# Kernel optimization log

Measured on AMD Instinct MI355X. Metric: run time of the kernel, lower is better.

Reference implementation:

```python
import jax, jax.numpy as jnp
import numpy as np

NEG = 0.01  # torch leaky_relu default slope


def conv1d(x, w, pad):
    # x: [B, C, L], w: [O, I, K], stride 1, no bias (as in FC-STGNN extractor)
    return jax.lax.conv_general_dilated(x, w, (1,), [(pad, pad)], dimension_numbers=('NCH', 'OIH', 'NCH'))


def maxpool2(x):
    # MaxPool1d(kernel=2, stride=2, padding=1); torch pads with -inf for max
    return jax.lax.reduce_window(x, -jnp.inf, jax.lax.max, (1, 1, 2), (1, 1, 2), ((0, 0), (0, 0), (1, 1)))


def pos_encoding(n, d):
    # standard sinusoidal PE table, rows 0..n-1 (n <= max_len=5000)
    pos = jnp.arange(n, dtype=jnp.float32)[:, None]
    div = jnp.exp(jnp.arange(0, d, 2, dtype=jnp.float32) * (-float(np.log(10000.0)) / d))
    pe = jnp.zeros((n, d), jnp.float32)
    pe = pe.at[:, 0::2].set(jnp.sin(pos * div))
    pe = pe.at[:, 1::2].set(jnp.cos(pos * div))
    return pe


def mpnn_block(x, gw, gb, bng, bnb, tw, tb):
    # GraphConvpoolMPNN_block_v6 with time_length=1, time_window_size=1, stride=1:
    # one window, decay mask = ones, mean-pool over the size-1 time window is identity.
    bs, two_h, N = x.shape
    X = x.reshape(bs, N, two_h)                                   # (bs*num_windows, num_node*tw, input_dim)
    h = X @ gw + gb                                               # Dot_Graph_Construction mapping
    adj = jnp.einsum('bnd,bmd->bnm', h, h)                        # dot-product adjacency
    eye = jnp.eye(N, dtype=X.dtype)
    adj = jax.nn.leaky_relu(adj - eye * 1e8, NEG)
    adj = jax.nn.softmax(adj, axis=-1) + eye
    Xb = X * bng + bnb                                            # BatchNorm1d eval (running mean 0 / var 1)
    out = jax.nn.leaky_relu(jnp.einsum('bnm,bmd->bnd', adj, Xb) @ tw + tb, NEG)  # MPNN_mk k=1
    return out                                                    # [bs, N, hidden]


def setup_inputs() -> dict:
    key = jax.random.key(0)
    ks = jax.random.split(key, 20)
    bs, D, N = 4, 128, 1024
    H, OUT, KS = 64, 32, 8        # lstmhidden_dim, lstmout_dim, conv_kernel
    HID = 64                      # hidden_dim
    TWOH = 2 * HID
    CONV_OUT = 18
    NCLS = 6
    f32 = jnp.float32
    rn = lambda k, s, sc: jax.random.normal(k, s, f32) * sc
    return {
        'x_enc': rn(ks[0], (bs, D, N), 1.0),
        'x_mark_enc': rn(ks[1], (bs, D, 4), 1.0),
        'x_dec': rn(ks[2], (bs, D // 2, N), 1.0),
        'x_mark_dec': rn(ks[3], (bs, D // 2, 4), 1.0),
        'conv_w1': rn(ks[4], (H, 1, KS), 1.0 / np.sqrt(KS)),
        'bn1_g': jnp.ones((H,), f32), 'bn1_b': jnp.zeros((H,), f32),
        'conv_w2': rn(ks[5], (2 * H, H, KS), 1.0 / np.sqrt(H * KS)),
        'bn2_g': jnp.ones((2 * H,), f32), 'bn2_b': jnp.zeros((2 * H,), f32),
        'conv_w3': rn(ks[6], (OUT, 2 * H, KS), 1.0 / np.sqrt(2 * H * KS)),
        'bn3_g': jnp.ones((OUT,), f32), 'bn3_b': jnp.zeros((OUT,), f32),
        'map2_w': rn(ks[7], (OUT * CONV_OUT, TWOH), 1.0 / np.sqrt(OUT * CONV_OUT)),
        'map2_b': jnp.zeros((TWOH,), f32),
        'map2_bn_g': jnp.ones((TWOH,), f32), 'map2_bn_b': jnp.zeros((TWOH,), f32),
        'g1_w': rn(ks[8], (TWOH, TWOH), 1.0 / np.sqrt(TWOH)), 'g1_b': jnp.zeros((TWOH,), f32),
        'm1_bn_g': jnp.ones((TWOH,), f32), 'm1_bn_b': jnp.zeros((TWOH,), f32),
        't1_w': rn(ks[9], (TWOH, HID), 1.0 / np.sqrt(TWOH)), 't1_b': jnp.zeros((HID,), f32),
        'g2_w': rn(ks[10], (TWOH, TWOH), 1.0 / np.sqrt(TWOH)), 'g2_b': jnp.zeros((TWOH,), f32),
        'm2_bn_g': jnp.ones((TWOH,), f32), 'm2_bn_b': jnp.zeros((TWOH,), f32),
        't2_w': rn(ks[11], (TWOH, HID), 1.0 / np.sqrt(TWOH)), 't2_b': jnp.zeros((HID,), f32),
        'fc1_w': rn(ks[12], (HID * 2 * N, TWOH), 1.0 / np.sqrt(HID * 2 * N)), 'fc1_b': jnp.zeros((TWOH,), f32),
        'fc2_w': rn(ks[13], (TWOH, TWOH), 1.0 / np.sqrt(TWOH)), 'fc2_b': jnp.zeros((TWOH,), f32),
        'fc3_w': rn(ks[14], (TWOH, HID), 1.0 / np.sqrt(TWOH)), 'fc3_b': jnp.zeros((HID,), f32),
        'fc4_w': rn(ks[15], (HID, NCLS), 1.0 / np.sqrt(HID)), 'fc4_b': jnp.zeros((NCLS,), f32),
    }


def reference(x_enc, x_mark_enc, x_dec, x_mark_dec,
              conv_w1, bn1_g, bn1_b, conv_w2, bn2_g, bn2_b, conv_w3, bn3_g, bn3_b,
              map2_w, map2_b, map2_bn_g, map2_bn_b,
              g1_w, g1_b, m1_bn_g, m1_bn_b, t1_w, t1_b,
              g2_w, g2_b, m2_bn_g, m2_bn_b, t2_w, t2_b,
              fc1_w, fc1_b, fc2_w, fc2_b, fc3_w, fc3_b, fc4_w, fc4_b):
    bs, D, N = x_enc.shape
    k = conv_w1.shape[-1]
    # nonlin_map: 1D-CNN feature extractor over each (sample, node) signal
    a = jnp.swapaxes(x_enc.reshape(bs * N, D, 1), 1, 2)           # [bs*N, 1, D]
    a = maxpool2(jax.nn.relu(conv1d(a, conv_w1, k // 2) * bn1_g[None, :, None] + bn1_b[None, :, None]))
    a = maxpool2(jax.nn.relu(conv1d(a, conv_w2, 4) * bn2_g[None, :, None] + bn2_b[None, :, None]))
    a = maxpool2(jax.nn.relu(conv1d(a, conv_w3, 4) * bn3_g[None, :, None] + bn3_b[None, :, None]))
    a = a.reshape(bs * N, -1)                                     # [bs*N, lstmout_dim*conv_out]
    # nonlin_map2: Linear + BatchNorm1d (eval mode affine)
    a = (a @ map2_w + map2_b) * map2_bn_g + map2_bn_b             # [bs*N, 2h]
    two_h = a.shape[-1]
    # positional encoding with the exact reshape/transpose traffic of the torch forward
    x = jnp.swapaxes(a.reshape(bs, N, two_h), 1, 2).reshape(bs * N, two_h)
    x = x + pos_encoding(bs * N, two_h)
    x = jnp.swapaxes(x.reshape(bs, N, two_h), 1, 2)               # [bs, 2h, N]
    # two graph MPNN branches
    o1 = mpnn_block(x, g1_w, g1_b, m1_bn_g, m1_bn_b, t1_w, t1_b)
    o2 = mpnn_block(x, g2_w, g2_b, m2_bn_g, m2_bn_b, t2_w, t2_b)
    f = jnp.concatenate([o1.reshape(bs, -1), o2.reshape(bs, -1)], axis=-1)
    # MLP head
    f = jax.nn.relu(f @ fc1_w + fc1_b)
    f = jax.nn.relu(f @ fc2_w + fc2_b)
    f = jax.nn.relu(f @ fc3_w + fc3_b)
    return f @ fc4_w + fc4_b                                      # [bs, n_class]
```

## Files before the change

kernel.cpp:

```cpp
#include <hip/hip_runtime.h>
#include <hip/hip_bf16.h>
#include <math.h>

#define NEG 0.01f
__device__ __forceinline__ float lrelu(float v){ return v > 0.f ? v : NEG*v; }
__device__ __forceinline__ float frelu(float v){ return v > 0.f ? v : 0.f; }

typedef __attribute__((ext_vector_type(8))) short bf16x8;
typedef __attribute__((ext_vector_type(4))) float f32x4;

__device__ __forceinline__ unsigned short f2bf(float x){
    unsigned int u = __float_as_uint(x);
    unsigned int r = (u + 0x7FFFu + ((u>>16)&1u)) >> 16;
    return (unsigned short)r;
}
__device__ __forceinline__ float bf2f(unsigned short h){
    return __uint_as_float(((unsigned int)h) << 16);
}
__device__ __forceinline__ unsigned short F2B(float x){
    __hip_bfloat16 h = __float2bfloat16(x);
    return *reinterpret_cast<unsigned short*>(&h);
}

__global__ __launch_bounds__(256) void k_prep(const float* __restrict__ w2, const float* __restrict__ w3,
    const float* __restrict__ m2w, const float* __restrict__ t1w, const float* __restrict__ t2w,
    unsigned short* __restrict__ w2s, unsigned short* __restrict__ w3s, unsigned short* __restrict__ m2wbT,
    unsigned short* __restrict__ twThi, unsigned short* __restrict__ twTlo)
{
    int gid = blockIdx.x*256 + threadIdx.x;
    if (gid < 73728) {
        int j = gid / 576, f = gid % 576;
        m2wbT[gid] = f2bf(m2w[f*128 + j]);
    }
    if (gid < 65536) {
        int jj = gid & 7, q = (gid>>3)&3, o = (gid>>5)&127, ks = (gid>>12)&1, k = gid>>13;
        int c = ks*32 + q*8 + jj;
        w2s[gid] = f2bf(w2[o*512 + c*8 + k]);
    }
    if (gid < 32768) {
        int jj = gid & 7, q = (gid>>3)&3, o = (gid>>5)&31, ks = (gid>>10)&3, k = gid>>12;
        int c = ks*32 + q*8 + jj;
        w3s[gid] = f2bf(w3[o*1024 + c*8 + k]);
    }
    if (gid < 16384) {
        int d = gid & 127, e = (gid>>7)&63, br = gid>>13;
        float x = (br ? t2w : t1w)[d*64 + e];
        unsigned short hh = f2bf(x);
        twThi[gid] = hh;
        twTlo[gid] = f2bf(x - bf2f(hh));
    }
}

__global__ __launch_bounds__(256) void k_conv(
    const float* __restrict__ xenc,
    const float* __restrict__ w1, const float* __restrict__ g1, const float* __restrict__ b1,
    const unsigned short* __restrict__ w2s, const float* __restrict__ g2, const float* __restrict__ b2,
    const unsigned short* __restrict__ w3s, const float* __restrict__ g3, const float* __restrict__ b3,
    unsigned short* __restrict__ aflatG)
{
    __shared__ __align__(16) unsigned char smraw[22208];
    float* sigp = (float*)smraw;
    unsigned short* p1T = (unsigned short*)(smraw + 576);
    unsigned short* p2T = (unsigned short*)(smraw + 10304);
    unsigned short* astage = (unsigned short*)(smraw + 21056);

    const int t = threadIdx.x;
    const int s = blockIdx.x;

    {
        unsigned int* zz = (unsigned int*)(smraw + 576);
        for (int i = t; i < 5120; i += 256) zz[i] = 0u;
        if (t < 144) sigp[t] = 0.f;
    }
    __syncthreads();
    if (t < 128) sigp[4 + t] = xenc[(size_t)s*128 + t];
    __syncthreads();

    {
        const int c = t & 63, qg = t >> 6;
        float wr[8];
        #pragma unroll
        for (int k = 0; k < 8; ++k) wr[k] = w1[c*8 + k];
        const float g = g1[c], b = b1[c];
        const int qs = qg*17;
        float win[9];
        {
            int base = 2*qs - 1;
            #pragma unroll
            for (int x = 0; x < 9; ++x) win[x] = (base + x >= 0) ? sigp[base + x] : 0.f;
        }
        #pragma unroll
        for (int j = 0; j < 17; ++j) {
            int q = qs + j;
            float s0 = 0.f, s1 = 0.f;
            #pragma unroll
            for (int k = 0; k < 8; ++k) { s0 += win[k]*wr[k]; s1 += win[k+1]*wr[k]; }
            float v = frelu(s1*g + b);
            if (q > 0) v = fmaxf(v, frelu(s0*g + b));
            if (q < 65) {
                int row = q + 4;
                p1T[row*64 + (((c>>3) ^ (row&7))<<3) + (c&7)] = F2B(v);
            }
            #pragma unroll
            for (int x = 0; x < 7; ++x) win[x] = win[x+2];
            win[7] = sigp[2*q + 8];
            win[8] = sigp[2*q + 9];
        }
    }
    __syncthreads();

    {
        const int wv = t >> 6, l = t & 63, lg = l >> 4, lr = l & 15;
        const int pbase = ((lr & 7) << 1) + (lr >> 3) - 1;
        const int o0 = (wv*2 + 0)*16 + lr;
        const int o1 = (wv*2 + 1)*16 + lr;
        f32x4 acc[2][5] = {};
        #pragma unroll
        for (int k = 0; k < 8; ++k) {
            const int rk = pbase + k;
            const int b0 = rk*64 + ((lg ^ (rk & 7)) << 3);
            #pragma unroll
            for (int ks = 0; ks < 2; ++ks) {
                bf16x8 af0 = *(const bf16x8*)(w2s + ((((k*2 + ks)*128 + o0)*4 + lg)<<3));
                bf16x8 af1 = *(const bf16x8*)(w2s + ((((k*2 + ks)*128 + o1)*4 + lg)<<3));
                const unsigned short* bp = p1T + (ks ? (b0 ^ 32) : b0);
                #pragma unroll
                for (int nt = 0; nt < 5; ++nt) {
                    bf16x8 bfv = *(const bf16x8*)(bp + nt*1024);
                    acc[0][nt] = __builtin_amdgcn_mfma_f32_16x16x32_bf16(af0, bfv, acc[0][nt], 0,0,0);
                    acc[1][nt] = __builtin_amdgcn_mfma_f32_16x16x32_bf16(af1, bfv, acc[1][nt], 0,0,0);
                }
            }
        }
        float ga[2][4], ba[2][4];
        #pragma unroll
        for (int oi = 0; oi < 2; ++oi)
            #pragma unroll
            for (int r = 0; r < 4; ++r) {
                int o = (wv*2 + oi)*16 + lg*4 + r;
                ga[oi][r] = g2[o]; ba[oi][r] = b2[o];
            }
        #pragma unroll
        for (int oi = 0; oi < 2; ++oi)
            #pragma unroll
            for (int nt = 0; nt < 5; ++nt) {
                int p = nt*16 + pbase;
                bool valid = (p >= 0) && (p <= 65);
                float vv[4];
                #pragma unroll
                for (int r = 0; r < 4; ++r) {
                    float v = frelu(acc[oi][nt][r]*ga[oi][r] + ba[oi][r]);
                    vv[r] = valid ? v : -3.0e38f;
                }
                float pv[4];
                #pragma unroll
                for (int r = 0; r < 4; ++r) pv[r] = fmaxf(vv[r], __shfl_xor(vv[r], 8));
                int q = nt*8 + (lr & 7);
                if ((lr >> 3) == 0 && q < 34) {
                    int row2 = q + 4;
                    int o0e = (wv*2 + oi)*16 + lg*4;
                    uint2 pk;
                    pk.x = (unsigned int)F2B(pv[0]) | ((unsigned int)F2B(pv[1]) << 16);
                    pk.y = (unsigned int)F2B(pv[2]) | ((unsigned int)F2B(pv[3]) << 16);
                    *(uint2*)&p2T[row2*128 + (((o0e>>3) ^ (row2&15))<<3) + (o0e&7)] = pk;
                }
            }
    }
    __syncthreads();

    {
        const int wv = t >> 6, l = t & 63, lg = l >> 4, lr = l & 15;
        const int ot = wv & 1, ntb = (wv >> 1) * 2;
        const int ncnt = (wv < 2) ? 2 : 1;
        const int pbase = ((lr & 7) << 1) + (lr >> 3) - 1;
        const int o = ot*16 + lr;
        f32x4 acc[2] = {};
        #pragma unroll
        for (int k = 0; k < 8; ++k) {
            const int rk = pbase + k;
            const int r15 = rk & 15;
            const int c2 = r15 >> 2;
            const int base0 = rk*128 + ((lg ^ (r15 & 3)) << 3) + ntb*2048;
            #pragma unroll
            for (int ks = 0; ks < 4; ++ks) {
                bf16x8 af = *(const bf16x8*)(w3s + ((((k*4 + ks)*32 + o)*4 + lg)<<3));
                const int bb = base0 + (((ks ^ c2) & 3) << 5);
                #pragma unroll
                for (int ni = 0; ni < 2; ++ni) {
                    if (ni < ncnt) {
                        int off = bb + ni*2048;
                        off = off > 5368 ? 5368 : off;
                        bf16x8 bfv = *(const bf16x8*)(p2T + off);
                        acc[ni] = __builtin_amdgcn_mfma_f32_16x16x32_bf16(af, bfv, acc[ni], 0,0,0);
                    }
                }
            }
        }
        float g3v[4], b3v[4];
        #pragma unroll
        for (int r = 0; r < 4; ++r) {
            int oe = ot*16 + lg*4 + r;
            g3v[r] = g3[oe]; b3v[r] = b3[oe];
        }
        #pragma unroll
        for (int ni = 0; ni < 2; ++ni) if (ni < ncnt) {
            int p = (ntb + ni)*16 + pbase;
            bool valid = (p >= 0) && (p <= 34);
            float vv[4];
            #pragma unroll
            for (int r = 0; r < 4; ++r) {
                float v = frelu(acc[ni][r]*g3v[r] + b3v[r]);
                vv[r] = valid ? v : -3.0e38f;
            }
            float pv[4];
            #pragma unroll
            for (int r = 0; r < 4; ++r) pv[r] = fmaxf(vv[r], __shfl_xor(vv[r], 8));
            int q = (ntb + ni)*8 + (lr & 7);
            if ((lr >> 3) == 0 && q < 18) {
                #pragma unroll
                for (int r = 0; r < 4; ++r)
                    astage[(ot*16 + lg*4 + r)*18 + q] = F2B(pv[r]);
            }
        }
    }
    __syncthreads();

    for (int idx = t; idx < 576; idx += 256)
        aflatG[(size_t)s*576 + idx] = astage[idx];
}

__global__ __launch_bounds__(256) void k_map2(const unsigned short* __restrict__ aflatG,
    const unsigned short* __restrict__ m2wbT,
    const float* __restrict__ m2b, const float* __restrict__ m2g, const float* __restrict__ m2bb,
    float* __restrict__ a2)
{
    const int t = threadIdx.x, wv = t>>6, l = t&63, lg = l>>4, lr = l&15;
    const int s0 = blockIdx.x*64;
    f32x4 acc[8] = {};
    for (int ks = 0; ks < 18; ++ks) {
        bf16x8 a = *(const bf16x8*)(aflatG + (size_t)(s0 + wv*16 + lr)*576 + ks*32 + lg*8);
        #pragma unroll
        for (int nt = 0; nt < 8; ++nt) {
            bf16x8 b = *(const bf16x8*)(m2wbT + (size_t)(nt*16 + lr)*576 + ks*32 + lg*8);
            acc[nt] = __builtin_amdgcn_mfma_f32_16x16x32_bf16(a, b, acc[nt], 0,0,0);
        }
    }
    #pragma unroll
    for (int nt = 0; nt < 8; ++nt)
        #pragma unroll
        for (int r = 0; r < 4; ++r) {
            int s2 = s0 + wv*16 + lg*4 + r;
            int j = nt*16 + lr;
            a2[(size_t)s2*128 + j] = (acc[nt][r] + m2b[j]) * m2g[j] + m2bb[j];
        }
}

__global__ __launch_bounds__(256) void k_buildx(const float* __restrict__ a2, float* __restrict__ X)
{
    __shared__ double dvt[64];
    const int t = threadIdx.x;
    if (t < 64) dvt[t] = exp((double)(2*t) * (-9.210340371976184/128.0));
    __syncthreads();
    int e = blockIdx.x*256 + t;
    int b = e >> 17;
    int r = e & 131071;
    int i = r >> 7, d = r & 127;
    int row = b*1024 + (d & 7)*128 + (i >> 3);
    int col = (i & 7)*16 + (d >> 3);
    float v = a2[row*128 + col];
    int per = b*1024 + (i & 7)*128 + d;
    int pc  = i >> 3;
    double ang = (double)per * dvt[pc >> 1];
    const double TWO_PI = 6.283185307179586476925287;
    double kk = floor(ang * (1.0/TWO_PI) + 0.5);
    float red = (float)(ang - kk * TWO_PI);
    float pe = (pc & 1) ? __cosf(red) : __sinf(red);
    X[e] = v + pe;
}

__global__ __launch_bounds__(256) void k_hmat(const float* __restrict__ X,
    const float* __restrict__ g1w, const float* __restrict__ g1b,
    const float* __restrict__ g2w, const float* __restrict__ g2b,
    unsigned short* __restrict__ Hbhi1, unsigned short* __restrict__ Hblo1,
    unsigned short* __restrict__ Hbhi2, unsigned short* __restrict__ Hblo2)
{
    const int br = blockIdx.y;
    const float* gw = br ? g2w : g1w;
    const float* gb = br ? g2b : g1b;
    unsigned short* Hh = br ? Hbhi2 : Hbhi1;
    unsigned short* Hl = br ? Hblo2 : Hblo1;
    int e = blockIdx.x*256 + threadIdx.x;
    int srow = e >> 7, j = e & 127;
    const float* xr = X + (size_t)srow*128;
    float acc = gb[j];
    for (int k = 0; k < 128; ++k) acc += xr[k] * gw[k*128 + j];
    unsigned short hh = f2bf(acc);
    Hh[e] = hh;
    Hl[e] = f2bf(acc - bf2f(hh));
}

__global__ __launch_bounds__(256) void k_scores(
    const unsigned short* __restrict__ Hbhi1, const unsigned short* __restrict__ Hblo1,
    const unsigned short* __restrict__ Hbhi2, const unsigned short* __restrict__ Hblo2,
    float* __restrict__ S1, float* __restrict__ S2)
{
    __shared__ __align__(16) unsigned short HiH[64*64];
    __shared__ __align__(16) unsigned short HiL[64*64];
    __shared__ __align__(16) unsigned short HjH[64*64];
    __shared__ __align__(16) unsigned short HjL[64*64];
    const int z = blockIdx.z;
    const int b = z & 3, br = z >> 2;
    const unsigned short* Hbhi = br ? Hbhi2 : Hbhi1;
    const unsigned short* Hblo = br ? Hblo2 : Hblo1;
    float* S = br ? S2 : S1;
    const int i0 = blockIdx.y * 64, j0 = blockIdx.x * 64;
    const int t = threadIdx.x;
    const int w = t >> 6, l = t & 63, lr = l & 15, h = l >> 4;
    const size_t hb = (size_t)b * 1024 * 128;

    f32x4 acc[4] = {};
    for (int kh = 0; kh < 2; ++kh) {
        __syncthreads();
        #pragma unroll
        for (int it = 0; it < 4; ++it) {
            int g = it*256 + t;
            int mat = g >> 9;
            int gg = g & 511;
            int row = gg >> 3, ch = gg & 7;
            int base0 = mat ? j0 : i0;
            size_t src = hb + (size_t)(base0 + row)*128 + kh*64 + ch*8;
            uint4 vh = *(const uint4*)(Hbhi + src);
            uint4 vl = *(const uint4*)(Hblo + src);
            int sw = ch ^ (row & 7);
            unsigned short* dh = (mat ? HjH : HiH) + row*64 + sw*8;
            unsigned short* dl = (mat ? HjL : HiL) + row*64 + sw*8;
            *(uint4*)dh = vh;
            *(uint4*)dl = vl;
        }
        __syncthreads();
        #pragma unroll
        for (int kc = 0; kc < 2; ++kc) {
            int swA = (((kc*4 + h) ^ (lr & 7)) << 3);
            bf16x8 ah = *(const bf16x8*)&HiH[(w*16 + lr)*64 + swA];
            bf16x8 al = *(const bf16x8*)&HiL[(w*16 + lr)*64 + swA];
            #pragma unroll
            for (int jt = 0; jt < 4; ++jt) {
                bf16x8 bh = *(const bf16x8*)&HjH[(jt*16 + lr)*64 + swA];
                bf16x8 bl = *(const bf16x8*)&HjL[(jt*16 + lr)*64 + swA];
                acc[jt] = __builtin_amdgcn_mfma_f32_16x16x32_bf16(ah, bh, acc[jt], 0,0,0);
                acc[jt] = __builtin_amdgcn_mfma_f32_16x16x32_bf16(ah, bl, acc[jt], 0,0,0);
                acc[jt] = __builtin_amdgcn_mfma_f32_16x16x32_bf16(al, bh, acc[jt], 0,0,0);
            }
        }
    }
    float* Sb = S + (size_t)b*1024*1024;
    #pragma unroll
    for (int jt = 0; jt < 4; ++jt) {
        #pragma unroll
        for (int r = 0; r < 4; ++r) {
            int i = i0 + w*16 + h*4 + r;
            int j = j0 + jt*16 + lr;
            float x = acc[jt][r];
            if (i == j) x -= 1e8f;
            Sb[(size_t)i*1024 + j] = lrelu(x);
        }
    }
}

__global__ __launch_bounds__(256) void k_rowstat(const float* __restrict__ S1, const float* __restrict__ S2,
                                                 float* __restrict__ mrow, float* __restrict__ linv)
{
    __shared__ float red[256];
    const int y = blockIdx.y, i = blockIdx.x, t = threadIdx.x;
    const int b = y & 3, br = y >> 2;
    const float* row = (br ? S2 : S1) + (size_t)b*1024*1024 + (size_t)i*1024;
    float4 v = *(const float4*)&row[t*4];
    float mx = fmaxf(fmaxf(v.x,v.y), fmaxf(v.z,v.w));
    red[t] = mx; __syncthreads();
    for (int s2 = 128; s2 > 0; s2 >>= 1) { if (t < s2) red[t] = fmaxf(red[t], red[t+s2]); __syncthreads(); }
    mx = red[0]; __syncthreads();
    float e = (__expf(v.x-mx) + __expf(v.y-mx)) + (__expf(v.z-mx) + __expf(v.w-mx));
    red[t] = e; __syncthreads();
    for (int s2 = 128; s2 > 0; s2 >>= 1) { if (t < s2) red[t] += red[t+s2]; __syncthreads(); }
    if (t == 0) { mrow[y*1024 + i] = mx; linv[y*1024 + i] = 1.f / red[0]; }
}

__global__ __launch_bounds__(256) void k_xbbt(const float* __restrict__ X,
    const float* __restrict__ bng1, const float* __restrict__ bnb1,
    const float* __restrict__ bng2, const float* __restrict__ bnb2,
    unsigned short* __restrict__ XbbThi, unsigned short* __restrict__ XbbTlo)
{
    __shared__ float Xl[64][132];
    const int t = threadIdx.x;
    const int j0 = blockIdx.x*64, b = blockIdx.y, br = blockIdx.z;
    {
        int r2 = t >> 2, dseg = (t & 3)*32;
        const float* src = X + ((size_t)(b*1024 + j0 + r2))*128 + dseg;
        #pragma unroll
        for (int q = 0; q < 8; ++q) {
            float4 v = *(const float4*)(src + q*4);
            Xl[r2][dseg + q*4 + 0] = v.x;
            Xl[r2][dseg + q*4 + 1] = v.y;
            Xl[r2][dseg + q*4 + 2] = v.z;
            Xl[r2][dseg + q*4 + 3] = v.w;
        }
    }
    __syncthreads();
    const int d = t >> 1, seg = t & 1;
    const float g  = (br ? bng2 : bng1)[d];
    const float bb = (br ? bnb2 : bnb1)[d];
    unsigned short* dsth = XbbThi + (size_t)br*524288 + ((size_t)(b*128 + d))*1024 + j0 + seg*32;
    unsigned short* dstl = XbbTlo + (size_t)br*524288 + ((size_t)(b*128 + d))*1024 + j0 + seg*32;
    #pragma unroll
    for (int g8 = 0; g8 < 4; ++g8) {
        unsigned int hu[4], lu[4];
        #pragma unroll
        for (int q = 0; q < 4; ++q) {
            float v0 = Xl[seg*32 + g8*8 + 2*q    ][d]*g + bb;
            float v1 = Xl[seg*32 + g8*8 + 2*q + 1][d]*g + bb;
            unsigned short h0 = f2bf(v0), h1 = f2bf(v1);
            hu[q] = (unsigned int)h0 | ((unsigned int)h1 << 16);
            lu[q] = (unsigned int)f2bf(v0 - bf2f(h0)) | ((unsigned int)f2bf(v1 - bf2f(h1)) << 16);
        }
        *(uint4*)(dsth + g8*8) = make_uint4(hu[0],hu[1],hu[2],hu[3]);
        *(uint4*)(dstl + g8*8) = make_uint4(lu[0],lu[1],lu[2],lu[3]);
    }
}

__global__ __launch_bounds__(256) void k_attn(
    const unsigned short* __restrict__ Hbhi1, const unsigned short* __restrict__ Hblo1,
    const unsigned short* __restrict__ Hbhi2, const unsigned short* __restrict__ Hblo2,
    const float* __restrict__ X,
    const float* __restrict__ bng1, const float* __restrict__ bnb1,
    const float* __restrict__ bng2, const float* __restrict__ bnb2,
    const unsigned short* __restrict__ XbbThi, const unsigned short* __restrict__ XbbTlo,
    unsigned short* __restrict__ Phi, unsigned short* __restrict__ Plo)
{
    __shared__ __align__(16) unsigned char lbuf[33280];
    const int t = threadIdx.x, w = t >> 6, l = t & 63, lr = l & 15, h = l >> 4;
    unsigned short* ElH = (unsigned short*)(lbuf + w*4096);
    unsigned short* ElL = (unsigned short*)(lbuf + w*4096 + 2048);
    float* Pred = (float*)lbuf;
    float* mW = (float*)(lbuf + 32768);
    float* lW = (float*)(lbuf + 32768 + 256);

    const int i0 = blockIdx.x * 16;
    const int b  = blockIdx.y;
    const int br = blockIdx.z;
    const unsigned short* Hh = br ? Hbhi2 : Hbhi1;
    const unsigned short* Hl = br ? Hblo2 : Hblo1;
    const unsigned short* Bh = XbbThi + (size_t)br*524288 + (size_t)b*131072;
    const unsigned short* Bl = XbbTlo + (size_t)br*524288 + (size_t)b*131072;
    const float* bng = br ? bng2 : bng1;
    const float* bnb = br ? bnb2 : bnb1;
    const size_t hb = (size_t)b * 1024 * 128;

    bf16x8 ahi[4], alo[4];
    #pragma unroll
    for (int kc = 0; kc < 4; ++kc) {
        size_t aoff = hb + (size_t)(i0 + lr)*128 + kc*32 + h*8;
        ahi[kc] = *(const bf16x8*)(Hh + aoff);
        alo[kc] = *(const bf16x8*)(Hl + aoff);
    }

    float m[4] = {-3.0e38f,-3.0e38f,-3.0e38f,-3.0e38f};
    float lsum[4] = {};
    f32x4 pacc[8] = {};

    for (int ch = 0; ch < 4; ++ch) {
        const int jbase = w*256 + ch*64;
        float sv[4][4];
        float cmax[4] = {-3.0e38f,-3.0e38f,-3.0e38f,-3.0e38f};
        #pragma unroll
        for (int jt = 0; jt < 4; ++jt) {
            f32x4 c = {};
            #pragma unroll
            for (int kc = 0; kc < 4; ++kc) {
                size_t boff = hb + (size_t)(jbase + jt*16 + lr)*128 + kc*32 + h*8;
                bf16x8 bh_ = *(const bf16x8*)(Hh + boff);
                bf16x8 bl_ = *(const bf16x8*)(Hl + boff);
                c = __builtin_amdgcn_mfma_f32_16x16x32_bf16(ahi[kc], bh_, c, 0,0,0);
                c = __builtin_amdgcn_mfma_f32_16x16x32_bf16(ahi[kc], bl_, c, 0,0,0);
                c = __builtin_amdgcn_mfma_f32_16x16x32_bf16(alo[kc], bh_, c, 0,0,0);
            }
            #pragma unroll
            for (int r = 0; r < 4; ++r) {
                float x = c[r];
                int ig = i0 + h*4 + r;
                int jg = jbase + jt*16 + lr;
                if (ig == jg) x -= 1e8f;
                x = lrelu(x);
                sv[jt][r] = x;
                cmax[r] = fmaxf(cmax[r], x);
            }
        }
        #pragma unroll
        for (int r = 0; r < 4; ++r) {
            cmax[r] = fmaxf(cmax[r], __shfl_xor(cmax[r], 1));
            cmax[r] = fmaxf(cmax[r], __shfl_xor(cmax[r], 2));
            cmax[r] = fmaxf(cmax[r], __shfl_xor(cmax[r], 4));
            cmax[r] = fmaxf(cmax[r], __shfl_xor(cmax[r], 8));
        }
        float scale[4];
        #pragma unroll
        for (int r = 0; r < 4; ++r) {
            float mn = fmaxf(m[r], cmax[r]);
            scale[r] = __expf(m[r] - mn);
            m[r] = mn;
        }
        float csum[4] = {};
        #pragma unroll
        for (int jt = 0; jt < 4; ++jt)
            #pragma unroll
            for (int r = 0; r < 4; ++r) {
                float e = __expf(sv[jt][r] - m[r]);
                csum[r] += e;
                unsigned short eh = f2bf(e);
                unsigned short el = f2bf(e - bf2f(eh));
                int ip = h*4 + r;
                int jp = jt*16 + lr;
                int addr = ip*64 + (((jp>>3) ^ (ip&7))<<3) + (jp&7);
                ElH[addr] = eh;
                ElL[addr] = el;
            }
        #pragma unroll
        for (int r = 0; r < 4; ++r) {
            csum[r] += __shfl_xor(csum[r], 1);
            csum[r] += __shfl_xor(csum[r], 2);
            csum[r] += __shfl_xor(csum[r], 4);
            csum[r] += __shfl_xor(csum[r], 8);
            lsum[r] = lsum[r]*scale[r] + csum[r];
        }
        #pragma unroll
        for (int dt = 0; dt < 8; ++dt)
            #pragma unroll
            for (int r = 0; r < 4; ++r) pacc[dt][r] *= scale[r];
        #pragma unroll
        for (int kc = 0; kc < 2; ++kc) {
            int swA = (((kc*4 + h) ^ (lr & 7)) << 3);
            bf16x8 eh8 = *(const bf16x8*)&ElH[lr*64 + swA];
            bf16x8 el8 = *(const bf16x8*)&ElL[lr*64 + swA];
            #pragma unroll
            for (int dt = 0; dt < 8; ++dt) {
                size_t boff = (size_t)(dt*16 + lr)*1024 + jbase + kc*32 + h*8;
                bf16x8 bh_ = *(const bf16x8*)(Bh + boff);
                bf16x8 bl_ = *(const bf16x8*)(Bl + boff);
                pacc[dt] = __builtin_amdgcn_mfma_f32_16x16x32_bf16(eh8, bh_, pacc[dt], 0,0,0);
                pacc[dt] = __builtin_amdgcn_mfma_f32_16x16x32_bf16(eh8, bl_, pacc[dt], 0,0,0);
                pacc[dt] = __builtin_amdgcn_mfma_f32_16x16x32_bf16(el8, bh_, pacc[dt], 0,0,0);
            }
        }
    }

    __syncthreads();
    #pragma unroll
    for (int dt = 0; dt < 8; ++dt)
        #pragma unroll
        for (int r = 0; r < 4; ++r)
            Pred[w*2048 + (h*4 + r)*128 + dt*16 + lr] = pacc[dt][r];
    if (lr == 0) {
        #pragma unroll
        for (int r = 0; r < 4; ++r) {
            mW[w*16 + h*4 + r] = m[r];
            lW[w*16 + h*4 + r] = lsum[r];
        }
    }
    __syncthreads();

    {
        int i = t >> 4, d0 = (t & 15) * 8;
        float m0 = mW[i], m1 = mW[16 + i], m2 = mW[32 + i], m3 = mW[48 + i];
        float ms = fmaxf(fmaxf(m0, m1), fmaxf(m2, m3));
        float e0 = __expf(m0 - ms), e1 = __expf(m1 - ms);
        float e2 = __expf(m2 - ms), e3 = __expf(m3 - ms);
        float ls = lW[i]*e0 + lW[16+i]*e1 + lW[32+i]*e2 + lW[48+i]*e3;
        float inv = 1.f / ls;
        unsigned int ph[4], pl[4];
        #pragma unroll
        for (int q2 = 0; q2 < 4; ++q2) {
            unsigned short hh0, hh1, ll0, ll1;
            #pragma unroll
            for (int half = 0; half < 2; ++half) {
                int d = d0 + 2*q2 + half;
                float P = Pred[i*128 + d]*e0 + Pred[2048 + i*128 + d]*e1
                        + Pred[4096 + i*128 + d]*e2 + Pred[6144 + i*128 + d]*e3;
                float xv = X[((size_t)(b*1024 + i0 + i))*128 + d] * bng[d] + bnb[d];
                float pv = P*inv + xv;
                unsigned short hh = f2bf(pv);
                unsigned short ll = f2bf(pv - bf2f(hh));
                if (half == 0) { hh0 = hh; ll0 = ll; } else { hh1 = hh; ll1 = ll; }
            }
            ph[q2] = (unsigned int)hh0 | ((unsigned int)hh1 << 16);
            pl[q2] = (unsigned int)ll0 | ((unsigned int)ll1 << 16);
        }
        size_t off = ((size_t)(br*4096 + b*1024 + i0 + i))*128 + d0;
        *(uint4*)(Phi + off) = make_uint4(ph[0],ph[1],ph[2],ph[3]);
        *(uint4*)(Plo + off) = make_uint4(pl[0],pl[1],pl[2],pl[3]);
    }
}

__global__ __launch_bounds__(256) void k_pv(const float* __restrict__ S, const float* __restrict__ X,
                                            const float* __restrict__ bng, const float* __restrict__ bnb,
                                            const float* __restrict__ mrowG, const float* __restrict__ linvG,
                                            float* __restrict__ P)
{
    __shared__ __align__(16) float Sl[16*65];
    __shared__ __align__(16) float Xl[64*132];
    const int b = blockIdx.y, i0 = blockIdx.x*16, t = threadIdx.x;
    const int il = t >> 4, dg = t & 15;
    const int sj = t & 63, sil = t >> 6;
    const int xd = t & 127, xj = t >> 7;
    const float bg = bng[xd], bb = bnb[xd];
    float mr[4];
    #pragma unroll
    for (int m2 = 0; m2 < 4; ++m2) mr[m2] = mrowG[b*1024 + i0 + sil*4 + m2];
    float acc[8] = {};
    const float* Sb = S + (size_t)b*1024*1024;
    const float* Xb = X + (size_t)b*1024*128;
    for (int c = 0; c < 16; ++c) {
        int jb = c*64;
        __syncthreads();
        #pragma unroll
        for (int m2 = 0; m2 < 4; ++m2) {
            int r2 = sil*4 + m2;
            Sl[r2*65 + sj] = __expf(Sb[(size_t)(i0+r2)*1024 + jb + sj] - mr[m2]);
        }
        #pragma unroll
        for (int m2 = 0; m2 < 32; ++m2) {
            int jc = xj + 2*m2;
            Xl[jc*132 + xd] = Xb[(size_t)(jb+jc)*128 + xd] * bg + bb;
        }
        __syncthreads();
        for (int jc = 0; jc < 64; ++jc) {
            float sv = Sl[il*65 + jc];
            float4 x0 = *(const float4*)&Xl[jc*132 + dg*8];
            float4 x1 = *(const float4*)&Xl[jc*132 + dg*8 + 4];
            acc[0] += sv*x0.x; acc[1] += sv*x0.y; acc[2] += sv*x0.z; acc[3] += sv*x0.w;
            acc[4] += sv*x1.x; acc[5] += sv*x1.y; acc[6] += sv*x1.z; acc[7] += sv*x1.w;
        }
    }
    int i = i0 + il;
    float inv = linvG[b*1024 + i];
    const float* xr = Xb + (size_t)i*128 + dg*8;
    float* pr = P + (size_t)(b*1024 + i)*128 + dg*8;
    #pragma unroll
    for (int z = 0; z < 8; ++z) {
        float xv = xr[z] * bng[dg*8+z] + bnb[dg*8+z];
        pr[z] = acc[z]*inv + xv;
    }
}

__global__ __launch_bounds__(256) void k_tprojmm(
    const unsigned short* __restrict__ Phi, const unsigned short* __restrict__ Plo,
    const unsigned short* __restrict__ twThi, const unsigned short* __restrict__ twTlo,
    const float* __restrict__ t1b, const float* __restrict__ t2b,
    float* __restrict__ O)
{
    const int t = threadIdx.x, w = t>>6, l = t&63, lr = l&15, h = l>>4;
    const int r0 = blockIdx.x*16;
    const int br = r0 >> 12;
    f32x4 acc = {};
    #pragma unroll
    for (int kc = 0; kc < 4; ++kc) {
        size_t aoff = (size_t)(r0 + lr)*128 + kc*32 + h*8;
        bf16x8 ah = *(const bf16x8*)(Phi + aoff);
        bf16x8 al = *(const bf16x8*)(Plo + aoff);
        size_t boff = (size_t)(br*64 + w*16 + lr)*128 + kc*32 + h*8;
        bf16x8 bh = *(const bf16x8*)(twThi + boff);
        bf16x8 bl = *(const bf16x8*)(twTlo + boff);
        acc = __builtin_amdgcn_mfma_f32_16x16x32_bf16(ah, bh, acc, 0,0,0);
        acc = __builtin_amdgcn_mfma_f32_16x16x32_bf16(ah, bl, acc, 0,0,0);
        acc = __builtin_amdgcn_mfma_f32_16x16x32_bf16(al, bh, acc, 0,0,0);
    }
    const float* tb = br ? t2b : t1b;
    float tbe = tb[w*16 + lr];
    int rowLocal0 = r0 & 4095;
    #pragma unroll
    for (int r = 0; r < 4; ++r) {
        int row = rowLocal0 + h*4 + r;
        O[(size_t)br*262144 + (size_t)row*64 + w*16 + lr] = lrelu(acc[r] + tbe);
    }
}

__global__ __launch_bounds__(256) void k_tproj(const float* __restrict__ P, const float* __restrict__ tw,
                                               const float* __restrict__ tb, float* __restrict__ O)
{
    int idx = blockIdx.x*256 + threadIdx.x;
    int srow = idx >> 6, e = idx & 63;
    const float* pr = P + (size_t)srow*128;
    float acc = tb[e];
    for (int d = 0; d < 128; ++d) acc += pr[d] * tw[d*64 + e];
    O[idx] = lrelu(acc);
}

__global__ __launch_bounds__(256) void k_fc1(const float* __restrict__ O1, const float* __restrict__ O2,
                                             const float* __restrict__ w, float* __restrict__ pbuf)
{
    __shared__ float red[4*512];
    const int t = threadIdx.x;
    const int wv = t >> 6, l = t & 63;
    const int gwid = blockIdx.x*4 + wv;
    float acc[4][2] = {};
    int base = gwid*64;
    for (int tt = 0; tt < 64; ++tt) {
        int row = base + tt;
        float2 wvv = *(const float2*)&w[(size_t)row*128 + l*2];
        #pragma unroll
        for (int b = 0; b < 4; ++b) {
            float fb = (row < 65536) ? O1[b*65536 + row] : O2[b*65536 + row - 65536];
            acc[b][0] += fb * wvv.x;
            acc[b][1] += fb * wvv.y;
        }
    }
    #pragma unroll
    for (int b = 0; b < 4; ++b) {
        red[wv*512 + b*128 + l*2]   = acc[b][0];
        red[wv*512 + b*128 + l*2+1] = acc[b][1];
    }
    __syncthreads();
    for (int rep = 0; rep < 2; ++rep) {
        int col = rep*256 + t;
        pbuf[(size_t)blockIdx.x*512 + col] = red[col] + red[512+col] + red[1024+col] + red[1536+col];
    }
}

__global__ __launch_bounds__(256) void k_red(const float* __restrict__ pbuf, float* __restrict__ pbuf2)
{
    int col = blockIdx.x*8 + (threadIdx.x >> 5);
    int lane = threadIdx.x & 31;
    float acc = 0.f;
    for (int it = 0; it < 16; ++it)
        acc += pbuf[(size_t)(lane + it*32)*512 + col];
    #pragma unroll
    for (int s2 = 16; s2 >= 1; s2 >>= 1) acc += __shfl_xor(acc, s2, 32);
    if (lane == 0) pbuf2[col] = acc;
}

__global__ __launch_bounds__(256) void k_head2(const float* __restrict__ pbuf2,
    const float* __restrict__ fc1b, const float* __restrict__ fc2w, const float* __restrict__ fc2b,
    const float* __restrict__ fc3w, const float* __restrict__ fc3b,
    const float* __restrict__ fc4w, const float* __restrict__ fc4b,
    float* __restrict__ out)
{
    __shared__ float r1[512], r2[512], r3[256];
    const int t = threadIdx.x;
    for (int rep = 0; rep < 2; ++rep) {
        int idx = rep*256 + t;
        r1[idx] = frelu(pbuf2[idx] + fc1b[idx & 127]);
    }
    __syncthreads();
    for (int rep = 0; rep < 2; ++rep) {
        int idx = rep*256 + t;
        int b = idx >> 7, j = idx & 127;
        float acc = fc2b[j];
        for (int k = 0; k < 128; ++k) acc += r1[b*128+k]*fc2w[k*128+j];
        r2[idx] = frelu(acc);
    }
    __syncthreads();
    {
        int b = t >> 6, e2 = t & 63;
        float acc = fc3b[e2];
        for (int k = 0; k < 128; ++k) acc += r2[b*128+k]*fc3w[k*64+e2];
        r3[t] = frelu(acc);
    }
    __syncthreads();
    if (t < 24) {
        int b = t/6, c = t%6;
        float acc = fc4b[c];
        for (int k = 0; k < 64; ++k) acc += r3[b*64+k]*fc4w[k*6+c];
        out[b*6+c] = acc;
    }
}

extern "C" void kernel_launch(void* const* d_in, const int* in_sizes, int n_in,
                              void* d_out, int out_size, void* d_ws, size_t ws_size,
                              hipStream_t stream)
{
    (void)in_sizes; (void)n_in; (void)out_size;
    const float* xenc = (const float*)d_in[0];
    const float* w1   = (const float*)d_in[4];
    const float* g1   = (const float*)d_in[5];
    const float* b1   = (const float*)d_in[6];
    const float* w2   = (const float*)d_in[7];
    const float* g2   = (const float*)d_in[8];
    const float* b2   = (const float*)d_in[9];
    const float* w3   = (const float*)d_in[10];
    const float* g3   = (const float*)d_in[11];
    const float* b3   = (const float*)d_in[12];
    const float* m2w  = (const float*)d_in[13];
    const float* m2b  = (const float*)d_in[14];
    const float* m2g  = (const float*)d_in[15];
    const float* m2bb = (const float*)d_in[16];
    const float* g1w  = (const float*)d_in[17];
    const float* g1b  = (const float*)d_in[18];
    const float* m1g  = (const float*)d_in[19];
    const float* m1b  = (const float*)d_in[20];
    const float* t1w  = (const float*)d_in[21];
    const float* t1b  = (const float*)d_in[22];
    const float* g2w  = (const float*)d_in[23];
    const float* g2bv = (const float*)d_in[24];
    const float* mm2g = (const float*)d_in[25];
    const float* mm2b = (const float*)d_in[26];
    const float* t2w  = (const float*)d_in[27];
    const float* t2b  = (const float*)d_in[28];
    const float* fc1w = (const float*)d_in[29];
    const float* fc1b = (const float*)d_in[30];
    const float* fc2w = (const float*)d_in[31];
    const float* fc2b = (const float*)d_in[32];
    const float* fc3w = (const float*)d_in[33];
    const float* fc3b = (const float*)d_in[34];
    const float* fc4w = (const float*)d_in[35];
    const float* fc4b = (const float*)d_in[36];

    char* ws = (char*)d_ws;
    float* a2   = (float*)(ws);
    float* X    = (float*)(ws + (2u<<20));
    unsigned short* Hbhi1 = (unsigned short*)(ws + (4u<<20));
    unsigned short* Hblo1 = (unsigned short*)(ws + (5u<<20));
    unsigned short* Hbhi2 = (unsigned short*)(ws);
    unsigned short* Hblo2 = (unsigned short*)(ws + (1u<<20));
    float* S1   = (float*)(ws + (6u<<20));
    unsigned short* aflatG = (unsigned short*)(ws + (6u<<20));
    unsigned short* w2s    = (unsigned short*)(ws + (6u<<20) + 5242880);
    unsigned short* w3s    = (unsigned short*)(ws + (6u<<20) + 5242880 + 131072);
    unsigned short* m2wbT  = (unsigned short*)(ws + (6u<<20) + 5242880 + 196608);
    float* pbuf2 = (float*)(ws + (6u<<20));

    if (ws_size >= ((size_t)49 << 20)) {
        unsigned short* Phi = (unsigned short*)(ws + (38u<<20));
        unsigned short* Plo = (unsigned short*)(ws + (40u<<20));
        float* O    = (float*)(ws + (42u<<20));
        float* pbuf = (float*)(ws + (44u<<20));
        unsigned short* twThi = (unsigned short*)(ws + (44u<<20) + 131072);
        unsigned short* twTlo = (unsigned short*)(ws + (44u<<20) + 196608);
        unsigned short* XbbThi = (unsigned short*)(ws + (45u<<20));
        unsigned short* XbbTlo = (unsigned short*)(ws + (47u<<20));
        float* O1 = O;
        float* O2 = O + 262144;

        k_prep<<<288, 256, 0, stream>>>(w2, w3, m2w, t1w, t2w, w2s, w3s, m2wbT, twThi, twTlo);
        k_conv<<<4096, 256, 0, stream>>>(xenc, w1,g1,b1, w2s,g2,b2, w3s,g3,b3, aflatG);
        k_map2<<<64, 256, 0, stream>>>(aflatG, m2wbT, m2b, m2g, m2bb, a2);
        k_buildx<<<2048, 256, 0, stream>>>(a2, X);
        k_hmat<<<dim3(2048,2), 256, 0, stream>>>(X, g1w, g1b, g2w, g2bv,
                                                 Hbhi1, Hblo1, Hbhi2, Hblo2);
        k_xbbt<<<dim3(16,4,2), 256, 0, stream>>>(X, m1g, m1b, mm2g, mm2b, XbbThi, XbbTlo);
        k_attn<<<dim3(64,4,2), 256, 0, stream>>>(Hbhi1, Hblo1, Hbhi2, Hblo2, X,
                                                 m1g, m1b, mm2g, mm2b,
                                                 XbbThi, XbbTlo, Phi, Plo);
        k_tprojmm<<<512, 256, 0, stream>>>(Phi, Plo, twThi, twTlo, t1b, t2b, O);
        k_fc1 <<<512, 256, 0, stream>>>(O1, O2, fc1w, pbuf);
        k_red <<<64, 256, 0, stream>>>(pbuf, pbuf2);
        k_head2<<<1, 256, 0, stream>>>(pbuf2, fc1b, fc2w, fc2b, fc3w, fc3b, fc4w, fc4b, (float*)d_out);
    } else {
        float* P    = (float*)(ws + (22u<<20));
        float* O1   = (float*)(ws + (24u<<20));
        float* O2   = (float*)(ws + (25u<<20));
        float* pbuf = (float*)(ws + (26u<<20));
        float* mrow = (float*)(ws + (26u<<20));
        float* linv = (float*)(ws + (26u<<20) + 65536);
        unsigned short* twThi = (unsigned short*)(ws + (26u<<20) + 131072);
        unsigned short* twTlo = (unsigned short*)(ws + (26u<<20) + 196608);

        k_prep<<<288, 256, 0, stream>>>(w2, w3, m2w, t1w, t2w, w2s, w3s, m2wbT, twThi, twTlo);
        k_conv<<<4096, 256, 0, stream>>>(xenc, w1,g1,b1, w2s,g2,b2, w3s,g3,b3, aflatG);
        k_map2<<<64, 256, 0, stream>>>(aflatG, m2wbT, m2b, m2g, m2bb, a2);
        k_buildx<<<2048, 256, 0, stream>>>(a2, X);
        k_hmat<<<dim3(2048,2), 256, 0, stream>>>(X, g1w, g1b, g2w, g2bv,
                                                 Hbhi1, Hblo1, Hbhi2, Hblo2);
        k_scores <<<dim3(16,16,4), 256, 0, stream>>>(Hbhi1, Hblo1, Hbhi1, Hblo1, S1, S1);
        k_rowstat<<<dim3(1024,4), 256, 0, stream>>>(S1, S1, mrow, linv);
        k_pv     <<<dim3(64,4), 256, 0, stream>>>(S1, X, m1g, m1b, mrow, linv, P);
        k_tproj  <<<1024, 256, 0, stream>>>(P, t1w, t1b, O1);
        k_scores <<<dim3(16,16,4), 256, 0, stream>>>(Hbhi2, Hblo2, Hbhi2, Hblo2, S1, S1);
        k_rowstat<<<dim3(1024,4), 256, 0, stream>>>(S1, S1, mrow, linv);
        k_pv     <<<dim3(64,4), 256, 0, stream>>>(S1, X, mm2g, mm2b, mrow, linv, P);
        k_tproj  <<<1024, 256, 0, stream>>>(P, t2w, t2b, O2);
        k_fc1 <<<512, 256, 0, stream>>>(O1, O2, fc1w, pbuf);
        k_red <<<64, 256, 0, stream>>>(pbuf, pbuf2);
        k_head2<<<1, 256, 0, stream>>>(pbuf2, fc1b, fc2w, fc2b, fc3w, fc3b, fc4w, fc4b, (float*)d_out);
    }
}
```

Measured before the change: 261.1 us.

## Process two sequences per conv block to reuse weight fragments

The fused conv kernel now handles two input sequences per workgroup, halving the grid. Weight A-fragments for conv2 and conv3 are loaded once and reused across both sequences' MFMAs, and the shared-memory buffers are doubled. This cuts global weight loads and per-block setup overhead, at the cost of doubled LDS use (about 44KB) and more accumulator registers, which may reduce occupancy.

```diff
diff --git a/kernel.cpp b/kernel.cpp
--- a/kernel.cpp
+++ b/kernel.cpp
@@ -58,22 +58,29 @@
     const unsigned short* __restrict__ w3s, const float* __restrict__ g3, const float* __restrict__ b3,
     unsigned short* __restrict__ aflatG)
 {
-    __shared__ __align__(16) unsigned char smraw[22208];
-    float* sigp = (float*)smraw;
-    unsigned short* p1T = (unsigned short*)(smraw + 576);
-    unsigned short* p2T = (unsigned short*)(smraw + 10304);
-    unsigned short* astage = (unsigned short*)(smraw + 21056);
+    __shared__ __align__(16) unsigned char smraw[44416];
+    float* sigp0 = (float*)smraw;
+    float* sigp1 = (float*)(smraw + 576);
+    unsigned short* p1T0 = (unsigned short*)(smraw + 1152);
+    unsigned short* p1T1 = (unsigned short*)(smraw + 10880);
+    unsigned short* p2T0 = (unsigned short*)(smraw + 20608);
+    unsigned short* p2T1 = (unsigned short*)(smraw + 31360);
+    unsigned short* ast0 = (unsigned short*)(smraw + 42112);
+    unsigned short* ast1 = (unsigned short*)(smraw + 43264);
 
     const int t = threadIdx.x;
-    const int s = blockIdx.x;
+    const int s0 = blockIdx.x*2;
 
     {
-        unsigned int* zz = (unsigned int*)(smraw + 576);
-        for (int i = t; i < 5120; i += 256) zz[i] = 0u;
-        if (t < 144) sigp[t] = 0.f;
-    }
-    __syncthreads();
-    if (t < 128) sigp[4 + t] = xenc[(size_t)s*128 + t];
+        unsigned int* zz = (unsigned int*)(smraw + 1152);
+        for (int i = t; i < 10240; i += 256) zz[i] = 0u;
+        if (t < 144) { sigp0[t] = 0.f; sigp1[t] = 0.f; }
+    }
+    __syncthreads();
+    if (t < 128) {
+        sigp0[4 + t] = xenc[(size_t)s0*128 + t];
+        sigp1[4 + t] = xenc[(size_t)(s0+1)*128 + t];
+    }
     __syncthreads();
 
     {
@@ -83,28 +90,41 @@
         for (int k = 0; k < 8; ++k) wr[k] = w1[c*8 + k];
         const float g = g1[c], b = b1[c];
         const int qs = qg*17;
-        float win[9];
+        float winA[9], winB[9];
         {
             int base = 2*qs - 1;
             #pragma unroll
-            for (int x = 0; x < 9; ++x) win[x] = (base + x >= 0) ? sigp[base + x] : 0.f;
+            for (int x = 0; x < 9; ++x) {
+                bool ok = (base + x >= 0);
+                winA[x] = ok ? sigp0[base + x] : 0.f;
+                winB[x] = ok ? sigp1[base + x] : 0.f;
+            }
         }
         #pragma unroll
         for (int j = 0; j < 17; ++j) {
             int q = qs + j;
-            float s0 = 0.f, s1 = 0.f;
-            #pragma unroll
-            for (int k = 0; k < 8; ++k) { s0 += win[k]*wr[k]; s1 += win[k+1]*wr[k]; }
-            float v = frelu(s1*g + b);
-            if (q > 0) v = fmaxf(v, frelu(s0*g + b));
+            float a0 = 0.f, a1 = 0.f, b0 = 0.f, b1 = 0.f;
+            #pragma unroll
+            for (int k = 0; k < 8; ++k) {
+                a0 += winA[k]*wr[k];  a1 += winA[k+1]*wr[k];
+                b0 += winB[k]*wr[k];  b1 += winB[k+1]*wr[k];
+            }
+            float vA = frelu(a1*g + b);
+            float vB = frelu(b1*g + b);
+            if (q > 0) {
+                vA = fmaxf(vA, frelu(a0*g + b));
+                vB = fmaxf(vB, frelu(b0*g + b));
+            }
             if (q < 65) {
                 int row = q + 4;
-                p1T[row*64 + (((c>>3) ^ (row&7))<<3) + (c&7)] = F2B(v);
-            }
-            #pragma unroll
-            for (int x = 0; x < 7; ++x) win[x] = win[x+2];
-            win[7] = sigp[2*q + 8];
-            win[8] = sigp[2*q + 9];
+                int addr = row*64 + (((c>>3) ^ (row&7))<<3) + (c&7);
+                p1T0[addr] = F2B(vA);
+                p1T1[addr] = F2B(vB);
+            }
+            #pragma unroll
+            for (int x = 0; x < 7; ++x) { winA[x] = winA[x+2]; winB[x] = winB[x+2]; }
+            winA[7] = sigp0[2*q + 8];  winA[8] = sigp0[2*q + 9];
+            winB[7] = sigp1[2*q + 8];  winB[8] = sigp1[2*q + 9];
         }
     }
     __syncthreads();
@@ -114,7 +134,7 @@
         const int pbase = ((lr & 7) << 1) + (lr >> 3) - 1;
         const int o0 = (wv*2 + 0)*16 + lr;
         const int o1 = (wv*2 + 1)*16 + lr;
-        f32x4 acc[2][5] = {};
+        f32x4 acc[2][5][2] = {};
         #pragma unroll
         for (int k = 0; k < 8; ++k) {
             const int rk = pbase + k;
@@ -123,12 +143,17 @@
             for (int ks = 0; ks < 2; ++ks) {
                 bf16x8 af0 = *(const bf16x8*)(w2s + ((((k*2 + ks)*128 + o0)*4 + lg)<<3));
                 bf16x8 af1 = *(const bf16x8*)(w2s + ((((k*2 + ks)*128 + o1)*4 + lg)<<3));
-                const unsigned short* bp = p1T + (ks ? (b0 ^ 32) : b0);
+                const int boff = ks ? (b0 ^ 32) : b0;
+                const unsigned short* bpA = p1T0 + boff;
+                const unsigned short* bpB = p1T1 + boff;
                 #pragma unroll
                 for (int nt = 0; nt < 5; ++nt) {
-                    bf16x8 bfv = *(const bf16x8*)(bp + nt*1024);
-                    acc[0][nt] = __builtin_amdgcn_mfma_f32_16x16x32_bf16(af0, bfv, acc[0][nt], 0,0,0);
-                    acc[1][nt] = __builtin_amdgcn_mfma_f32_16x16x32_bf16(af1, bfv, acc[1][nt], 0,0,0);
+                    bf16x8 bfA = *(const bf16x8*)(bpA + nt*1024);
+                    bf16x8 bfB = *(const bf16x8*)(bpB + nt*1024);
+                    acc[0][nt][0] = __builtin_amdgcn_mfma_f32_16x16x32_bf16(af0, bfA, acc[0][nt][0], 0,0,0);
+                    acc[1][nt][0] = __builtin_amdgcn_mfma_f32_16x16x32_bf16(af1, bfA, acc[1][nt][0], 0,0,0);
+                    acc[0][nt][1] = __builtin_amdgcn_mfma_f32_16x16x32_bf16(af0, bfB, acc[0][nt][1], 0,0,0);
+                    acc[1][nt][1] = __builtin_amdgcn_mfma_f32_16x16x32_bf16(af1, bfB, acc[1][nt][1], 0,0,0);
                 }
             }
         }
@@ -141,30 +166,34 @@
                 ga[oi][r] = g2[o]; ba[oi][r] = b2[o];
             }
         #pragma unroll
-        for (int oi = 0; oi < 2; ++oi)
-            #pragma unroll
-            for (int nt = 0; nt < 5; ++nt) {
-                int p = nt*16 + pbase;
-                bool valid = (p >= 0) && (p <= 65);
-                float vv[4];
+        for (int sg = 0; sg < 2; ++sg) {
+            unsigned short* p2T = sg ? p2T1 : p2T0;
+            #pragma unroll
+            for (int oi = 0; oi < 2; ++oi)
                 #pragma unroll
-                for (int r = 0; r < 4; ++r) {
-                    float v = frelu(acc[oi][nt][r]*ga[oi][r] + ba[oi][r]);
-                    vv[r] = valid ? v : -3.0e38f;
+                for (int nt = 0; nt < 5; ++nt) {
+                    int p = nt*16 + pbase;
+                    bool valid = (p >= 0) && (p <= 65);
+                    float vv[4];
+                    #pragma unroll
+                    for (int r = 0; r < 4; ++r) {
+                        float v = frelu(acc[oi][nt][sg][r]*ga[oi][r] + ba[oi][r]);
+                        vv[r] = valid ? v : -3.0e38f;
+                    }
+                    float pv[4];
+                    #pragma unroll
+                    for (int r = 0; r < 4; ++r) pv[r] = fmaxf(vv[r], __shfl_xor(vv[r], 8));
+                    int q = nt*8 + (lr & 7);
+                    if ((lr >> 3) == 0 && q < 34) {
+                        int row2 = q + 4;
+                        int o0e = (wv*2 + oi)*16 + lg*4;
+                        uint2 pk;
+                        pk.x = (unsigned int)F2B(pv[0]) | ((unsigned int)F2B(pv[1]) << 16);
+                        pk.y = (unsigned int)F2B(pv[2]) | ((unsigned int)F2B(pv[3]) << 16);
+                        *(uint2*)&p2T[row2*128 + (((o0e>>3) ^ (row2&15))<<3) + (o0e&7)] = pk;
+                    }
                 }
-                float pv[4];
-                #pragma unroll
-                for (int r = 0; r < 4; ++r) pv[r] = fmaxf(vv[r], __shfl_xor(vv[r], 8));
-                int q = nt*8 + (lr & 7);
-                if ((lr >> 3) == 0 && q < 34) {
-                    int row2 = q + 4;
-                    int o0e = (wv*2 + oi)*16 + lg*4;
-                    uint2 pk;
-                    pk.x = (unsigned int)F2B(pv[0]) | ((unsigned int)F2B(pv[1]) << 16);
-                    pk.y = (unsigned int)F2B(pv[2]) | ((unsigned int)F2B(pv[3]) << 16);
-                    *(uint2*)&p2T[row2*128 + (((o0e>>3) ^ (row2&15))<<3) + (o0e&7)] = pk;
-                }
-            }
+        }
     }
     __syncthreads();
 
@@ -174,7 +203,7 @@
         const int ncnt = (wv < 2) ? 2 : 1;
         const int pbase = ((lr & 7) << 1) + (lr >> 3) - 1;
         const int o = ot*16 + lr;
-        f32x4 acc[2] = {};
+        f32x4 acc[2][2] = {};
         #pragma unroll
         for (int k = 0; k < 8; ++k) {
             const int rk = pbase + k;
@@ -190,8 +219,10 @@
                     if (ni < ncnt) {
                         int off = bb + ni*2048;
                         off = off > 5368 ? 5368 : off;
-                        bf16x8 bfv = *(const bf16x8*)(p2T + off);
-                        acc[ni] = __builtin_amdgcn_mfma_f32_16x16x32_bf16(af, bfv, acc[ni], 0,0,0);
+                        bf16x8 bfA = *(const bf16x8*)(p2T0 + off);
+                        bf16x8 bfB = *(const bf16x8*)(p2T1 + off);
+                        acc[ni][0] = __builtin_amdgcn_mfma_f32_16x16x32_bf16(af, bfA, acc[ni][0], 0,0,0);
+                        acc[ni][1] = __builtin_amdgcn_mfma_f32_16x16x32_bf16(af, bfB, acc[ni][1], 0,0,0);
                     }
                 }
             }
@@ -203,30 +234,37 @@
             g3v[r] = g3[oe]; b3v[r] = b3[oe];
         }
         #pragma unroll
-        for (int ni = 0; ni < 2; ++ni) if (ni < ncnt) {
-            int p = (ntb + ni)*16 + pbase;
-            bool valid = (p >= 0) && (p <= 34);
-            float vv[4];
-            #pragma unroll
-            for (int r = 0; r < 4; ++r) {
-                float v = frelu(acc[ni][r]*g3v[r] + b3v[r]);
-                vv[r] = valid ? v : -3.0e38f;
-            }
-            float pv[4];
-            #pragma unroll
-            for (int r = 0; r < 4; ++r) pv[r] = fmaxf(vv[r], __shfl_xor(vv[r], 8));
-            int q = (ntb + ni)*8 + (lr & 7);
-            if ((lr >> 3) == 0 && q < 18) {
+        for (int sg = 0; sg < 2; ++sg) {
+            unsigned short* ast = sg ? ast1 : ast0;
+            #pragma unroll
+            for (int ni = 0; ni < 2; ++ni) if (ni < ncnt) {
+                int p = (ntb + ni)*16 + pbase;
+                bool valid = (p >= 0) && (p <= 34);
+                float vv[4];
                 #pragma unroll
-                for (int r = 0; r < 4; ++r)
-                    astage[(ot*16 + lg*4 + r)*18 + q] = F2B(pv[r]);
-            }
-        }
-    }
-    __syncthreads();
-
-    for (int idx = t; idx < 576; idx += 256)
-        aflatG[(size_t)s*576 + idx] = astage[idx];
+                for (int r = 0; r < 4; ++r) {
+                    float v = frelu(acc[ni][sg][r]*g3v[r] + b3v[r]);
+                    vv[r] = valid ? v : -3.0e38f;
+                }
+                float pv[4];
+                #pragma unroll
+                for (int r = 0; r < 4; ++r) pv[r] = fmaxf(vv[r], __shfl_xor(vv[r], 8));
+                int q = (ntb + ni)*8 + (lr & 7);
+                if ((lr >> 3) == 0 && q < 18) {
+                    #pragma unroll
+                    for (int r = 0; r < 4; ++r)
+                        ast[(ot*16 + lg*4 + r)*18 + q] = F2B(pv[r]);
+                }
+            }
+        }
+    }
+    __syncthreads();
+
+    for (int idx = t; idx < 1152; idx += 256) {
+        int sg = idx >= 576;
+        int e = idx - sg*576;
+        aflatG[(size_t)(s0 + sg)*576 + e] = (sg ? ast1 : ast0)[e];
+    }
 }
 
 __global__ __launch_bounds__(256) void k_map2(const unsigned short* __restrict__ aflatG,
@@ -839,7 +877,7 @@
         float* O2 = O + 262144;
 
         k_prep<<<288, 256, 0, stream>>>(w2, w3, m2w, t1w, t2w, w2s, w3s, m2wbT, twThi, twTlo);
-        k_conv<<<4096, 256, 0, stream>>>(xenc, w1,g1,b1, w2s,g2,b2, w3s,g3,b3, aflatG);
+        k_conv<<<2048, 256, 0, stream>>>(xenc, w1,g1,b1, w2s,g2,b2, w3s,g3,b3, aflatG);
         k_map2<<<64, 256, 0, stream>>>(aflatG, m2wbT, m2b, m2g, m2bb, a2);
         k_buildx<<<2048, 256, 0, stream>>>(a2, X);
         k_hmat<<<dim3(2048,2), 256, 0, stream>>>(X, g1w, g1b, g2w, g2bv,
@@ -863,7 +901,7 @@
         unsigned short* twTlo = (unsigned short*)(ws + (26u<<20) + 196608);
 
         k_prep<<<288, 256, 0, stream>>>(w2, w3, m2w, t1w, t2w, w2s, w3s, m2wbT, twThi, twTlo);
-        k_conv<<<4096, 256, 0, stream>>>(xenc, w1,g1,b1, w2s,g2,b2, w3s,g3,b3, aflatG);
+        k_conv<<<2048, 256, 0, stream>>>(xenc, w1,g1,b1, w2s,g2,b2, w3s,g3,b3, aflatG);
         k_map2<<<64, 256, 0, stream>>>(aflatG, m2wbT, m2b, m2g, m2bb, a2);
         k_buildx<<<2048, 256, 0, stream>>>(a2, X);
         k_hmat<<<dim3(2048,2), 256, 0, stream>>>(X, g1w, g1b, g2w, g2bv,
```

After: 267.9 us (median of 2 runs). 2.6% more time.
